# Performance work log

Hardware: AMD Instinct MI355X
Metric: run time of the kernel (lower is better)

The kernel has to match this reference:

```python
import jax, jax.numpy as jnp
import numpy as np


def setup_inputs() -> dict:
    key = jax.random.key(0)
    ks = jax.random.split(key, 5)
    b, n_q, n_kv = 16, 128, 4096
    query_dim, context_dim, heads, dim_head = 1024, 1024, 16, 64
    inner = heads * dim_head
    x = jax.random.normal(ks[0], (b, n_q, query_dim), dtype=jnp.float32)
    context = jax.random.normal(ks[1], (b, n_kv, context_dim), dtype=jnp.float32)
    # Linear weights stored as (in, out); scaled like default torch init magnitude
    Wq = jax.random.normal(ks[2], (query_dim, inner), dtype=jnp.float32) * (query_dim ** -0.5)
    Wkv = jax.random.normal(ks[3], (context_dim, 2 * inner), dtype=jnp.float32) * (context_dim ** -0.5)
    Wout = jax.random.normal(ks[4], (inner, query_dim), dtype=jnp.float32) * (inner ** -0.5)
    bout = jnp.zeros((query_dim,), dtype=jnp.float32)
    return {"x": x, "context": context, "Wq": Wq, "Wkv": Wkv, "Wout": Wout, "bout": bout}


def reference(x, context, Wq, Wkv, Wout, bout):
    heads, dim_head = 16, 64
    b, n_q, _ = x.shape
    n_kv = context.shape[1]
    scale = dim_head ** -0.5

    q = x @ Wq                       # [b, n_q, h*d]
    kv = context @ Wkv               # [b, n_kv, 2*h*d]
    k, v = jnp.split(kv, 2, axis=-1)

    def split_heads(t):
        bb, n, _ = t.shape
        return t.reshape(bb, n, heads, dim_head).transpose(0, 2, 1, 3)  # [b, h, n, d]

    q, k, v = map(split_heads, (q, k, v))

    # mask[i, j] = (i - (j % n_q) == 0)  -> query i attends keys j with j % n_q == i
    i_idx = jnp.arange(n_q)[:, None]
    j_idx = jnp.arange(n_kv)[None, :]
    mask = (j_idx % n_q) == i_idx      # [n_q, n_kv] bool

    sim = jnp.einsum('bhid,bhjd->bhij', q, k) * scale
    max_neg = -jnp.finfo(sim.dtype).max
    sim = jnp.where(mask[None, None, :, :], sim, max_neg)
    attn = jax.nn.softmax(sim, axis=-1)
    out = jnp.einsum('bhij,bhjd->bhid', attn, v)   # [b, h, n_q, d]
    out = out.transpose(0, 2, 1, 3).reshape(b, n_q, heads * dim_head)
    return out @ Wout + bout
```

## Files before the change

kernel.cpp:

```cpp
#include <hip/hip_runtime.h>
#include <hip/hip_bf16.h>

typedef __attribute__((ext_vector_type(8))) short short8;
typedef __attribute__((ext_vector_type(4))) float floatx4;

__device__ __forceinline__ unsigned short f32_to_bf16(float f) {
    unsigned int u = __builtin_bit_cast(unsigned int, f);
    u = (u + 0x7FFFu + ((u >> 16) & 1u)) >> 16;
    return (unsigned short)u;
}
__device__ __forceinline__ unsigned int pack_bf16x2(float lo, float hi) {
    return (unsigned int)f32_to_bf16(lo) | ((unsigned int)f32_to_bf16(hi) << 16);
}
__device__ __forceinline__ void async_load16(const unsigned short* g, unsigned short* l) {
    __builtin_amdgcn_global_load_lds(
        (const __attribute__((address_space(1))) void*)g,
        (__attribute__((address_space(3))) void*)l, 16, 0, 0);
}

__device__ __forceinline__ void transpose_tile(
    const float* __restrict__ W, int src_ld, int n_off,
    unsigned short* __restrict__ Wt, int dst_ld, int nb, int kb, int tid) {
    __shared__ float tile[32][33];
    int n0 = nb * 32, k0 = kb * 32;
    int tx = tid & 31, ty = tid >> 5;
#pragma unroll
    for (int p = 0; p < 4; ++p) {
        int r = ty + 8 * p;
        tile[r][tx] = W[(long)(k0 + r) * src_ld + n_off + n0 + tx];
    }
    __syncthreads();
#pragma unroll
    for (int p = 0; p < 4; ++p) {
        int r = ty + 8 * p;
        Wt[(long)(n0 + r) * dst_ld + k0 + tx] = f32_to_bf16(tile[tx][r]);
    }
}

__device__ __forceinline__ void cast8(
    const float* __restrict__ src, unsigned short* __restrict__ dst) {
    floatx4 a = *(const floatx4*)src;
    floatx4 b = *(const floatx4*)(src + 4);
    uint4 p;
    p.x = pack_bf16x2(a[0], a[1]); p.y = pack_bf16x2(a[2], a[3]);
    p.z = pack_bf16x2(b[0], b[1]); p.w = pack_bf16x2(b[2], b[3]);
    *(uint4*)dst = p;
}

__device__ __forceinline__ void cast8_nt(
    const float* __restrict__ src, unsigned short* __restrict__ dst) {
    floatx4 a = __builtin_nontemporal_load((const floatx4*)src);
    floatx4 b = __builtin_nontemporal_load((const floatx4*)(src + 4));
    uint4 p;
    p.x = pack_bf16x2(a[0], a[1]); p.y = pack_bf16x2(a[2], a[3]);
    p.z = pack_bf16x2(b[0], b[1]); p.w = pack_bf16x2(b[2], b[3]);
    *(uint4*)dst = p;
}

__global__ __launch_bounds__(256) void prep_kernel(
    const float* __restrict__ Wq, const float* __restrict__ Wkv,
    const float* __restrict__ Wout, const float* __restrict__ x,
    unsigned short* __restrict__ WqT, unsigned short* __restrict__ WkB,
    unsigned short* __restrict__ WvT, unsigned short* __restrict__ WoutT,
    unsigned short* __restrict__ xb) {
    int id = blockIdx.x, tid = threadIdx.x;
    if (id < 1024) { transpose_tile(Wq,   1024, 0,    WqT,   1024, id & 31, id >> 5, tid); return; }
    id -= 1024;
    if (id < 1024) { transpose_tile(Wkv,  2048, 1024, WvT,   1024, id & 31, id >> 5, tid); return; }
    id -= 1024;
    if (id < 1024) { transpose_tile(Wout, 1024, 0,    WoutT, 1024, id & 31, id >> 5, tid); return; }
    id -= 1024;
    if (id < 512) {
        long e = ((long)id * 256 + tid) * 8;
        long row = e >> 10, col = e & 1023;
        cast8(Wkv + row * 2048 + col, WkB + e);
        return;
    }
    id -= 512;
    { long e = ((long)id * 256 + tid) * 8; cast8(x + e, xb + e); }
}

__global__ __launch_bounds__(256, 4) void gemm64_kernel(
    const unsigned short* __restrict__ A, long sA, int lda,
    const unsigned short* __restrict__ Bt, long sB, int ldb,
    void* __restrict__ C, long sC, int ldc,
    const float* __restrict__ bias, int K, int out_bf16) {
    __shared__ unsigned short As[128 * 32];
    __shared__ unsigned short Bs[64 * 32];

    const int tid = threadIdx.x, wave = tid >> 6, lane = tid & 63;
    const int z = blockIdx.z;
    A  += (long)z * sA;
    Bt += (long)z * sB;
    const int m0 = blockIdx.y * 128, n0 = blockIdx.x * 64;

    floatx4 acc[2][4];
#pragma unroll
    for (int i = 0; i < 2; ++i)
#pragma unroll
        for (int j = 0; j < 4; ++j) acc[i][j] = (floatx4)0.0f;

    const int kofs = (lane & 3) * 8;
    const unsigned short* aAddr = A  + (long)(m0 + wave * 32 + (lane >> 2)) * lda + kofs;
    const unsigned short* bAddr = Bt + (long)(n0 + wave * 16 + (lane >> 2)) * ldb + kofs;
    unsigned short* asBase = &As[wave * 1024];
    unsigned short* bsBase = &Bs[wave * 512];

    const int frm = lane & 15, fk = (lane >> 4) * 8;

    for (int kk = 0; kk < K; kk += 32) {
        __syncthreads();
        async_load16(aAddr + kk,                  asBase);
        async_load16(aAddr + (long)16 * lda + kk, asBase + 512);
        async_load16(bAddr + kk,                  bsBase);
        __syncthreads();

        short8 afrag[2], bfrag[4];
#pragma unroll
        for (int rt = 0; rt < 2; ++rt)
            afrag[rt] = *(const short8*)&As[(wave * 32 + rt * 16 + frm) * 32 + fk];
#pragma unroll
        for (int ct = 0; ct < 4; ++ct)
            bfrag[ct] = *(const short8*)&Bs[(ct * 16 + frm) * 32 + fk];
#pragma unroll
        for (int rt = 0; rt < 2; ++rt)
#pragma unroll
            for (int ct = 0; ct < 4; ++ct)
                acc[rt][ct] = __builtin_amdgcn_mfma_f32_16x16x32_bf16(
                    afrag[rt], bfrag[ct], acc[rt][ct], 0, 0, 0);
    }

    const int orow0 = m0 + wave * 32 + (lane >> 4) * 4;
    const int ocol0 = n0 + (lane & 15);
    if (out_bf16) {
        unsigned short* Cb = (unsigned short*)C + (long)z * sC;
#pragma unroll
        for (int rt = 0; rt < 2; ++rt)
#pragma unroll
            for (int r = 0; r < 4; ++r) {
                long row = orow0 + rt * 16 + r;
#pragma unroll
                for (int ct = 0; ct < 4; ++ct)
                    Cb[row * ldc + ocol0 + ct * 16] = f32_to_bf16(acc[rt][ct][r]);
            }
    } else {
        float* Cf = (float*)C + (long)z * sC;
#pragma unroll
        for (int rt = 0; rt < 2; ++rt)
#pragma unroll
            for (int r = 0; r < 4; ++r) {
                long row = orow0 + rt * 16 + r;
#pragma unroll
                for (int ct = 0; ct < 4; ++ct) {
                    int col = ocol0 + ct * 16;
                    float v = acc[rt][ct][r];
                    if (bias) v += bias[col];
                    Cf[row * ldc + col] = v;
                }
            }
    }
}

__global__ __launch_bounds__(256, 4) void gemm64s_kernel(
    const unsigned short* __restrict__ A, long sA, int lda,
    const unsigned short* __restrict__ Bt, long sB, int ldb,
    void* __restrict__ C, long sC, int ldc,
    const float* __restrict__ bias, int K, int out_bf16) {
    __shared__ unsigned short As[64 * 32];
    __shared__ unsigned short Bs[64 * 32];

    const int tid = threadIdx.x, wave = tid >> 6, lane = tid & 63;
    const int z = blockIdx.z;
    A  += (long)z * sA;
    Bt += (long)z * sB;
    const int m0 = blockIdx.y * 64, n0 = blockIdx.x * 64;

    floatx4 acc[4];
#pragma unroll
    for (int j = 0; j < 4; ++j) acc[j] = (floatx4)0.0f;

    const int kofs = (lane & 3) * 8;
    const unsigned short* aAddr = A  + (long)(m0 + wave * 16 + (lane >> 2)) * lda + kofs;
    const unsigned short* bAddr = Bt + (long)(n0 + wave * 16 + (lane >> 2)) * ldb + kofs;
    unsigned short* asBase = &As[wave * 512];
    unsigned short* bsBase = &Bs[wave * 512];

    const int frm = lane & 15, fk = (lane >> 4) * 8;

    for (int kk = 0; kk < K; kk += 32) {
        __syncthreads();
        async_load16(aAddr + kk, asBase);
        async_load16(bAddr + kk, bsBase);
        __syncthreads();

        short8 afrag = *(const short8*)&As[(wave * 16 + frm) * 32 + fk];
        short8 bfrag[4];
#pragma unroll
        for (int ct = 0; ct < 4; ++ct)
            bfrag[ct] = *(const short8*)&Bs[(ct * 16 + frm) * 32 + fk];
#pragma unroll
        for (int ct = 0; ct < 4; ++ct)
            acc[ct] = __builtin_amdgcn_mfma_f32_16x16x32_bf16(
                afrag, bfrag[ct], acc[ct], 0, 0, 0);
    }

    const int orow0 = m0 + wave * 16 + (lane >> 4) * 4;
    const int ocol0 = n0 + (lane & 15);
    if (out_bf16) {
        unsigned short* Cb = (unsigned short*)C + (long)z * sC;
#pragma unroll
        for (int r = 0; r < 4; ++r) {
            long row = orow0 + r;
#pragma unroll
            for (int ct = 0; ct < 4; ++ct)
                Cb[row * ldc + ocol0 + ct * 16] = f32_to_bf16(acc[ct][r]);
        }
    } else {
        float* Cf = (float*)C + (long)z * sC;
#pragma unroll
        for (int r = 0; r < 4; ++r) {
            long row = orow0 + r;
#pragma unroll
            for (int ct = 0; ct < 4; ++ct) {
                int col = ocol0 + ct * 16;
                float v = acc[ct][r];
                if (bias) v += bias[col];
                Cf[row * ldc + col] = v;
            }
        }
    }
}

#define CLD 1032
__device__ __forceinline__ int swzb(int t, int c) {
    return t * (2 * CLD) + ((2 * c) ^ (((t >> 3) & 3) << 5));
}
__global__ __launch_bounds__(256, 2) void attn_fused_kernel(
    const float* __restrict__ ctx,
    const unsigned short* __restrict__ qt,
    unsigned short* __restrict__ wctx) {
    __shared__ unsigned short ctx_t[32 * CLD];
    __shared__ float sred[4 * 544];
    __shared__ unsigned short p_l[16 * 40];

    const int tid = threadIdx.x, wave = tid >> 6, lane = tid & 63;
    const int bi = blockIdx.x;
    const int b = bi >> 7, i = bi & 127;
    const int frm = lane & 15, fk = (lane >> 4) * 8;

    short8 af[8];
    const unsigned short* qbase =
        qt + (long)bi * 16384 + (long)frm * 1024 + wave * 256 + fk;
#pragma unroll
    for (int it = 0; it < 8; ++it) af[it] = *(const short8*)(qbase + it * 32);

#pragma unroll
    for (int rr = 0; rr < 16; ++rr) {
        int idx = rr * 2048 + tid * 8;
        int t = idx >> 10, c = idx & 1023;
        cast8_nt(ctx + ((long)b * 4096 + i + t * 128) * 1024 + c,
                 (unsigned short*)((char*)ctx_t + swzb(t, c)));
    }
    __syncthreads();

    floatx4 acc0 = (floatx4)0.0f, acc1 = (floatx4)0.0f;
    __builtin_amdgcn_s_setprio(1);
#pragma unroll
    for (int it = 0; it < 8; ++it) {
        int kk = wave * 256 + it * 32;
        short8 b0 = *(const short8*)((const char*)ctx_t + swzb(frm, kk + fk));
        short8 b1 = *(const short8*)((const char*)ctx_t + swzb(16 + frm, kk + fk));
        acc0 = __builtin_amdgcn_mfma_f32_16x16x32_bf16(af[it], b0, acc0, 0, 0, 0);
        acc1 = __builtin_amdgcn_mfma_f32_16x16x32_bf16(af[it], b1, acc1, 0, 0, 0);
    }
    __builtin_amdgcn_s_setprio(0);
#pragma unroll
    for (int r = 0; r < 4; ++r) {
        sred[wave * 544 + frm * 17 + (lane >> 4) * 4 + r]        = acc0[r];
        sred[wave * 544 + (16 + frm) * 17 + (lane >> 4) * 4 + r] = acc1[r];
    }
    __syncthreads();

    {
        const int h = wave * 4 + (lane >> 4);
        const int tg = lane & 15;
        const int i0 = tg * 17 + h, i1 = (16 + tg) * 17 + h;
        float s0 = (sred[i0] + sred[544 + i0] + sred[1088 + i0] + sred[1632 + i0]) * 0.125f;
        float s1 = (sred[i1] + sred[544 + i1] + sred[1088 + i1] + sred[1632 + i1]) * 0.125f;
        float m = fmaxf(s0, s1);
#pragma unroll
        for (int d = 1; d < 16; d <<= 1) m = fmaxf(m, __shfl_xor(m, d));
        float e0 = __expf(s0 - m), e1 = __expf(s1 - m);
        float den = e0 + e1;
#pragma unroll
        for (int d = 1; d < 16; d <<= 1) den += __shfl_xor(den, d);
        float inv = 1.0f / den;
        p_l[h * 40 + tg]      = f32_to_bf16(e0 * inv);
        p_l[h * 40 + 16 + tg] = f32_to_bf16(e1 * inv);
    }
    __syncthreads();

    short8 ap;
#pragma unroll
    for (int j = 0; j < 8; ++j) ap[j] = (short)p_l[frm * 40 + fk + j];

    unsigned short* wbase =
        wctx + (long)bi * 16384 + (long)frm * 1024 + (lane >> 4) * 4;
    __builtin_amdgcn_s_setprio(1);
#pragma unroll 4
    for (int nt = 0; nt < 16; ++nt) {
        int c0 = wave * 256 + nt * 16;
        short8 av;
#pragma unroll
        for (int j = 0; j < 8; ++j)
            av[j] = (short)*(const unsigned short*)
                        ((const char*)ctx_t + swzb(fk + j, c0 + frm));
        floatx4 wacc = __builtin_amdgcn_mfma_f32_16x16x32_bf16(
            av, ap, (floatx4)0.0f, 0, 0, 0);
        uint2 st;
        st.x = pack_bf16x2(wacc[0], wacc[1]);
        st.y = pack_bf16x2(wacc[2], wacc[3]);
        *(uint2*)(wbase + c0) = st;
    }
    __builtin_amdgcn_s_setprio(0);
}

extern "C" void kernel_launch(void* const* d_in, const int* in_sizes, int n_in,
                              void* d_out, int out_size, void* d_ws, size_t ws_size,
                              hipStream_t stream) {
    const float* x       = (const float*)d_in[0];
    const float* context = (const float*)d_in[1];
    const float* Wq      = (const float*)d_in[2];
    const float* Wkv     = (const float*)d_in[3];
    const float* Wout    = (const float*)d_in[4];
    const float* bout    = (const float*)d_in[5];
    float* out = (float*)d_out;

    char* ws = (char*)d_ws;
    unsigned short* WqT   = (unsigned short*)(ws);
    unsigned short* WkB   = (unsigned short*)(ws + (2ll  << 20));
    unsigned short* WvT   = (unsigned short*)(ws + (4ll  << 20));
    unsigned short* WoutT = (unsigned short*)(ws + (6ll  << 20));
    unsigned short* xb    = (unsigned short*)(ws + (8ll  << 20));
    unsigned short* qb    = (unsigned short*)(ws + (12ll << 20));
    unsigned short* aob   = (unsigned short*)(ws + (16ll << 20));
    unsigned short* qtb   = (unsigned short*)(ws + (32ll << 20));
    unsigned short* wctxb = (unsigned short*)(ws + (96ll << 20));

    prep_kernel<<<4608, 256, 0, stream>>>(Wq, Wkv, Wout, x, WqT, WkB, WvT, WoutT, xb);

    gemm64s_kernel<<<dim3(16, 32, 1), 256, 0, stream>>>(
        xb, 0, 1024, WqT, 0, 1024, qb, 0, 1024, nullptr, 1024, 1);
    gemm64_kernel<<<dim3(16, 16, 16), 256, 0, stream>>>(
        qb, 64, 1024, WkB, 64, 1024, qtb, 1024, 16384, nullptr, 64, 1);
    attn_fused_kernel<<<2048, 256, 0, stream>>>(context, qtb, wctxb);
    gemm64s_kernel<<<dim3(1, 32, 16), 256, 0, stream>>>(
        wctxb, 1024, 16384, WvT, (long)64 * 1024, 1024, aob, 64, 1024, nullptr, 1024, 1);
    gemm64s_kernel<<<dim3(16, 32, 1), 256, 0, stream>>>(
        aob, 0, 1024, WoutT, 0, 1024, out, 0, 1024, bout, 1024, 0);
}
```

Before: 454.0 us.

## Double-buffer GEMM tiles with XOR-swizzled LDS and 64-wide K steps

The small-tile GEMM now loads 64-wide K tiles into two LDS buffers with an XOR swizzle. It prefetches the next tile asynchronously while MFMAs run on the current one and raises wave priority around the math. The 128-row GEMM drops its K loop and loads a single 64-wide K tile, so it now assumes K equals 64. The aim is to hide global load latency, halve the barriers per K step and cut LDS bank conflicts. The cost is more LDS per block, which may lower occupancy, and the 128-row kernel silently depends on K being 64.

```diff
diff --git a/kernel.cpp b/kernel.cpp
--- a/kernel.cpp
+++ b/kernel.cpp
@@ -85,14 +85,14 @@
     const unsigned short* __restrict__ Bt, long sB, int ldb,
     void* __restrict__ C, long sC, int ldc,
     const float* __restrict__ bias, int K, int out_bf16) {
-    __shared__ unsigned short As[128 * 32];
-    __shared__ unsigned short Bs[64 * 32];
+    __shared__ unsigned short As[128 * 64];
+    __shared__ unsigned short Bs[64 * 64];
 
     const int tid = threadIdx.x, wave = tid >> 6, lane = tid & 63;
     const int z = blockIdx.z;
-    A  += (long)z * sA;
-    Bt += (long)z * sB;
     const int m0 = blockIdx.y * 128, n0 = blockIdx.x * 64;
+    const unsigned short* Ab = A  + (long)z * sA + (long)m0 * lda;
+    const unsigned short* Bb = Bt + (long)z * sB + (long)n0 * ldb;
 
     floatx4 acc[2][4];
 #pragma unroll
@@ -100,35 +100,42 @@
 #pragma unroll
         for (int j = 0; j < 4; ++j) acc[i][j] = (floatx4)0.0f;
 
-    const int kofs = (lane & 3) * 8;
-    const unsigned short* aAddr = A  + (long)(m0 + wave * 32 + (lane >> 2)) * lda + kofs;
-    const unsigned short* bAddr = Bt + (long)(n0 + wave * 16 + (lane >> 2)) * ldb + kofs;
-    unsigned short* asBase = &As[wave * 1024];
-    unsigned short* bsBase = &Bs[wave * 512];
-
-    const int frm = lane & 15, fk = (lane >> 4) * 8;
-
-    for (int kk = 0; kk < K; kk += 32) {
-        __syncthreads();
-        async_load16(aAddr + kk,                  asBase);
-        async_load16(aAddr + (long)16 * lda + kk, asBase + 512);
-        async_load16(bAddr + kk,                  bsBase);
-        __syncthreads();
-
-        short8 afrag[2], bfrag[4];
-#pragma unroll
-        for (int rt = 0; rt < 2; ++rt)
-            afrag[rt] = *(const short8*)&As[(wave * 32 + rt * 16 + frm) * 32 + fk];
-#pragma unroll
-        for (int ct = 0; ct < 4; ++ct)
-            bfrag[ct] = *(const short8*)&Bs[(ct * 16 + frm) * 32 + fk];
-#pragma unroll
-        for (int rt = 0; rt < 2; ++rt)
-#pragma unroll
-            for (int ct = 0; ct < 4; ++ct)
+#pragma unroll
+    for (int s = 0; s < 4; ++s) {
+        int E = s * 2048 + tid * 8;
+        int r = E >> 6, g = ((E >> 3) & 7) ^ (r & 7);
+        async_load16(Ab + (long)r * lda + g * 8, &As[s * 2048 + wave * 512]);
+    }
+#pragma unroll
+    for (int s = 0; s < 2; ++s) {
+        int E = s * 2048 + tid * 8;
+        int r = E >> 6, g = ((E >> 3) & 7) ^ (r & 7);
+        async_load16(Bb + (long)r * ldb + g * 8, &Bs[s * 2048 + wave * 512]);
+    }
+    __syncthreads();
+
+    const int frm = lane & 15, gq = lane >> 4;
+    __builtin_amdgcn_s_setprio(1);
+#pragma unroll
+    for (int ks = 0; ks < 2; ++ks) {
+        const int Ga = ks * 4 + gq;
+        short8 a[2];
+#pragma unroll
+        for (int rt = 0; rt < 2; ++rt) {
+            int Ra = wave * 32 + rt * 16 + frm;
+            a[rt] = *(const short8*)&As[Ra * 64 + ((Ga ^ (Ra & 7)) << 3)];
+        }
+#pragma unroll
+        for (int ct = 0; ct < 4; ++ct) {
+            int Rb = ct * 16 + frm;
+            short8 b = *(const short8*)&Bs[Rb * 64 + ((Ga ^ (Rb & 7)) << 3)];
+#pragma unroll
+            for (int rt = 0; rt < 2; ++rt)
                 acc[rt][ct] = __builtin_amdgcn_mfma_f32_16x16x32_bf16(
-                    afrag[rt], bfrag[ct], acc[rt][ct], 0, 0, 0);
-    }
+                    a[rt], b, acc[rt][ct], 0, 0, 0);
+        }
+    }
+    __builtin_amdgcn_s_setprio(0);
 
     const int orow0 = m0 + wave * 32 + (lane >> 4) * 4;
     const int ocol0 = n0 + (lane & 15);
@@ -166,42 +173,62 @@
     const unsigned short* __restrict__ Bt, long sB, int ldb,
     void* __restrict__ C, long sC, int ldc,
     const float* __restrict__ bias, int K, int out_bf16) {
-    __shared__ unsigned short As[64 * 32];
-    __shared__ unsigned short Bs[64 * 32];
+    __shared__ unsigned short As[2][64 * 64];
+    __shared__ unsigned short Bs[2][64 * 64];
 
     const int tid = threadIdx.x, wave = tid >> 6, lane = tid & 63;
     const int z = blockIdx.z;
-    A  += (long)z * sA;
-    Bt += (long)z * sB;
     const int m0 = blockIdx.y * 64, n0 = blockIdx.x * 64;
+    const unsigned short* Ab = A  + (long)z * sA + (long)m0 * lda;
+    const unsigned short* Bb = Bt + (long)z * sB + (long)n0 * ldb;
 
     floatx4 acc[4];
 #pragma unroll
     for (int j = 0; j < 4; ++j) acc[j] = (floatx4)0.0f;
 
-    const int kofs = (lane & 3) * 8;
-    const unsigned short* aAddr = A  + (long)(m0 + wave * 16 + (lane >> 2)) * lda + kofs;
-    const unsigned short* bAddr = Bt + (long)(n0 + wave * 16 + (lane >> 2)) * ldb + kofs;
-    unsigned short* asBase = &As[wave * 512];
-    unsigned short* bsBase = &Bs[wave * 512];
-
-    const int frm = lane & 15, fk = (lane >> 4) * 8;
-
-    for (int kk = 0; kk < K; kk += 32) {
+    const int frm = lane & 15, gq = lane >> 4;
+    const int E0 = tid * 8;
+
+    const int nt = K >> 6;
+    int cur = 0;
+#pragma unroll
+    for (int s = 0; s < 2; ++s) {
+        int E = s * 2048 + E0;
+        int r = E >> 6, g = ((E >> 3) & 7) ^ (r & 7);
+        async_load16(Ab + (long)r * lda + g * 8, &As[0][s * 2048 + wave * 512]);
+        async_load16(Bb + (long)r * ldb + g * 8, &Bs[0][s * 2048 + wave * 512]);
+    }
+
+    for (int t = 0; t < nt; ++t) {
         __syncthreads();
-        async_load16(aAddr + kk, asBase);
-        async_load16(bAddr + kk, bsBase);
-        __syncthreads();
-
-        short8 afrag = *(const short8*)&As[(wave * 16 + frm) * 32 + fk];
-        short8 bfrag[4];
-#pragma unroll
-        for (int ct = 0; ct < 4; ++ct)
-            bfrag[ct] = *(const short8*)&Bs[(ct * 16 + frm) * 32 + fk];
-#pragma unroll
-        for (int ct = 0; ct < 4; ++ct)
-            acc[ct] = __builtin_amdgcn_mfma_f32_16x16x32_bf16(
-                afrag, bfrag[ct], acc[ct], 0, 0, 0);
+        if (t + 1 < nt) {
+            int kk = (t + 1) << 6;
+#pragma unroll
+            for (int s = 0; s < 2; ++s) {
+                int E = s * 2048 + E0;
+                int r = E >> 6, g = ((E >> 3) & 7) ^ (r & 7);
+                async_load16(Ab + (long)r * lda + kk + g * 8,
+                             &As[cur ^ 1][s * 2048 + wave * 512]);
+                async_load16(Bb + (long)r * ldb + kk + g * 8,
+                             &Bs[cur ^ 1][s * 2048 + wave * 512]);
+            }
+        }
+        __builtin_amdgcn_s_setprio(1);
+#pragma unroll
+        for (int ks = 0; ks < 2; ++ks) {
+            const int Ga = ks * 4 + gq;
+            const int Ra = wave * 16 + frm;
+            short8 a = *(const short8*)&As[cur][Ra * 64 + ((Ga ^ (Ra & 7)) << 3)];
+#pragma unroll
+            for (int ct = 0; ct < 4; ++ct) {
+                int Rb = ct * 16 + frm;
+                short8 b = *(const short8*)&Bs[cur][Rb * 64 + ((Ga ^ (Rb & 7)) << 3)];
+                acc[ct] = __builtin_amdgcn_mfma_f32_16x16x32_bf16(
+                    a, b, acc[ct], 0, 0, 0);
+            }
+        }
+        __builtin_amdgcn_s_setprio(0);
+        cur ^= 1;
     }
 
     const int orow0 = m0 + wave * 16 + (lane >> 4) * 4;
```

After: 446.9 us. No clear change (-1.6%).
